# Kernel tuning notes

Hardware: AMD Instinct MI355X
Metric: run time of the kernel (lower is better)

The kernel has to match this reference:

```python
import jax, jax.numpy as jnp
import numpy as np

N = 100000      # nodes (max(content_indices)+1)
E = 1600000     # edges
TXT, VIS = 768, 512
IN = 128        # in_channels (already even)
FEAT = IN + 3   # feature_size = in_channels + 3 (ars)
HID, OUT, CAT = 128, 128, 2
NEG_SLOPE = 0.2


def setup_inputs() -> dict:
    key = jax.random.key(0)
    ks = jax.random.split(key, 20)
    p = lambda k, sh: jax.random.normal(k, sh, jnp.float32) * 0.02
    return {
        "image_features": jax.random.normal(ks[0], (N, VIS), jnp.float32),
        "text_features": jax.random.normal(ks[1], (N, TXT), jnp.float32),
        "content_indices": jnp.arange(N, dtype=jnp.int32),
        "gt_indices": jax.random.randint(ks[2], (N,), 0, 2, jnp.int32),
        "edges": jax.random.randint(ks[3], (E, 2), 0, N, jnp.int32),
        "ars": jax.random.uniform(ks[4], (N, 3), jnp.float32),
        # linear projections
        "Wi": p(ks[5], (VIS, IN // 2)), "bi": jnp.zeros((IN // 2,), jnp.float32),
        "Wt": p(ks[6], (TXT, IN // 2)), "bt": jnp.zeros((IN // 2,), jnp.float32),
        # GATConv layer 0: FEAT -> HID (heads=1)
        "W0": p(ks[7], (FEAT, HID)), "as0": p(ks[8], (HID,)), "ad0": p(ks[9], (HID,)),
        "b0": jnp.zeros((HID,), jnp.float32),
        # GATConv layer 1: HID -> OUT
        "W1": p(ks[10], (HID, OUT)), "as1": p(ks[11], (OUT,)), "ad1": p(ks[12], (OUT,)),
        "b1": jnp.zeros((OUT,), jnp.float32),
        "Wa": p(ks[13], (OUT, CAT)), "ba": jnp.zeros((CAT,), jnp.float32),
        "Wd": p(ks[14], (OUT, CAT)), "bd": jnp.zeros((CAT,), jnp.float32),
    }


def gat_conv(x, src, dst, W, att_src, att_dst, bias):
    """PyG GATConv, heads=1, add_self_loops=True, negative_slope=0.2."""
    h = x @ W                                    # [N, D]
    loop = jnp.arange(N, dtype=src.dtype)
    s = jnp.concatenate([src, loop])             # [E+N]
    d = jnp.concatenate([dst, loop])
    a_s = (h * att_src).sum(-1)                  # [N]
    a_d = (h * att_dst).sum(-1)
    e = jax.nn.leaky_relu(a_s[s] + a_d[d], NEG_SLOPE)   # [E+N]
    # segment softmax over incoming edges of each dst node
    e_max = jax.ops.segment_max(e, d, num_segments=N)
    ee = jnp.exp(e - e_max[d])
    denom = jax.ops.segment_sum(ee, d, num_segments=N)
    alpha = ee / (denom[d] + 1e-16)
    out = jax.ops.segment_sum(h[s] * alpha[:, None], d, num_segments=N)
    return out + bias


def reference(image_features, text_features, content_indices, gt_indices, edges, ars,
              Wi, bi, Wt, bt, W0, as0, ad0, b0, W1, as1, ad1, b1, Wa, ba, Wd, bd):
    img = image_features @ Wi + bi              # [N, IN//2]
    txt = text_features @ Wt + bt               # [N, IN//2]
    inp = jnp.concatenate([img, txt, ars], axis=1)   # [N, FEAT]
    node = jnp.zeros((N, FEAT), jnp.float32).at[content_indices].set(inp)
    node = jax.nn.gelu(node, approximate=False)
    src, dst = edges[:, 0], edges[:, 1]         # edge_index = edges.T
    h = gat_conv(node, src, dst, W0, as0, ad0, b0)
    h = jax.nn.relu(h)                          # PyG GAT inter-layer act
    h = gat_conv(h, src, dst, W1, as1, ad1, b1)
    out = jax.nn.gelu(h, approximate=False)     # [N, OUT]
    angles = out @ Wa + ba                      # [N, CAT]
    dists = out @ Wd + bd
    # per-edge tiny dot products (bmm of [E,1,C] x [E,C,1])
    ap = jnp.sum(angles[src] * angles[dst], axis=-1, keepdims=True)  # [E,1]
    dp = jnp.sum(dists[src] * dists[dst], axis=-1, keepdims=True)
    prediction = jnp.concatenate([ap, dp], axis=-1)   # [E, 2]
    return out, prediction
```

## Files before the change

### kernel.cpp

```cpp
#include <hip/hip_runtime.h>
#include <math.h>

#define N_NODES 100000
#define N_EDGES 1600000
#define FEATP 132
#define HID 128

__device__ __forceinline__ float geluf(float x) {
    return 0.5f * x * (1.0f + erff(x * 0.7071067811865475f));
}
__device__ __forceinline__ float leakyf(float x) {
    return x >= 0.0f ? x : 0.2f * x;
}
__device__ __forceinline__ float wave_reduce_max(float v) {
#pragma unroll
    for (int o = 32; o > 0; o >>= 1) v = fmaxf(v, __shfl_xor(v, o, 64));
    return v;
}
__device__ __forceinline__ float wave_reduce_sum(float v) {
#pragma unroll
    for (int o = 32; o > 0; o >>= 1) v += __shfl_xor(v, o, 64);
    return v;
}

template <int ACT>
__global__ __launch_bounds__(256) void gemm128(
    const float* __restrict__ A, int lda, int M, int K,
    const float* __restrict__ B, int ldb,
    const float* __restrict__ bias,
    float* __restrict__ C, int ldc, int colOff,
    const int* __restrict__ rowIdx)
{
    __shared__ float As[32][132];
    __shared__ float Bs[32][64];
    const int tid = threadIdx.x;
    const int m0 = blockIdx.x * 128;
    const int n0 = blockIdx.y * 64;
    const int tx = tid & 15, ty = tid >> 4;

    const int arow = tid >> 3;
    const int acol = (tid & 7) * 4;
    const int brow = tid >> 4;
    const int bcol = (tid & 15) * 4;

    float4 pa[4], pb[2];
    const int T = (K + 31) / 32;

    auto fetch = [&](int k0) {
#pragma unroll
        for (int i = 0; i < 4; ++i) {
            int row = m0 + i * 32 + arow;
            int k = k0 + acol;
            pa[i] = (row < M && k < K) ? *(const float4*)&A[(size_t)row * lda + k]
                                       : make_float4(0.f, 0.f, 0.f, 0.f);
        }
#pragma unroll
        for (int i = 0; i < 2; ++i) {
            int k = k0 + i * 16 + brow;
            pb[i] = (k < K) ? *(const float4*)&B[(size_t)k * ldb + n0 + bcol]
                            : make_float4(0.f, 0.f, 0.f, 0.f);
        }
    };

    float acc[8][4] = {};
    fetch(0);
    for (int t = 0; t < T; ++t) {
#pragma unroll
        for (int i = 0; i < 4; ++i) {
            int row = i * 32 + arow;
            As[acol + 0][row] = pa[i].x;
            As[acol + 1][row] = pa[i].y;
            As[acol + 2][row] = pa[i].z;
            As[acol + 3][row] = pa[i].w;
        }
#pragma unroll
        for (int i = 0; i < 2; ++i)
            *(float4*)&Bs[i * 16 + brow][bcol] = pb[i];
        __syncthreads();
        if (t + 1 < T) fetch((t + 1) * 32);
#pragma unroll
        for (int kk = 0; kk < 32; ++kk) {
            float4 a0 = *(const float4*)&As[kk][ty * 8];
            float4 a1 = *(const float4*)&As[kk][ty * 8 + 4];
            float4 b  = *(const float4*)&Bs[kk][tx * 4];
            float av[8] = {a0.x, a0.y, a0.z, a0.w, a1.x, a1.y, a1.z, a1.w};
            float bv[4] = {b.x, b.y, b.z, b.w};
#pragma unroll
            for (int i = 0; i < 8; ++i)
#pragma unroll
                for (int j = 0; j < 4; ++j)
                    acc[i][j] = fmaf(av[i], bv[j], acc[i][j]);
        }
        __syncthreads();
    }

#pragma unroll
    for (int i = 0; i < 8; ++i) {
        int row = m0 + ty * 8 + i;
        if (row >= M) continue;
        int orow = rowIdx ? rowIdx[row] : row;
        float4 v;
        float* vp = (float*)&v;
#pragma unroll
        for (int j = 0; j < 4; ++j) {
            float x = acc[i][j];
            if (bias) x += bias[n0 + tx * 4 + j];
            if (ACT == 1) x = geluf(x);
            vp[j] = x;
        }
        *(float4*)&C[(size_t)orow * ldc + colOff + n0 + tx * 4] = v;
    }
}

__global__ void ars_kernel(const float* __restrict__ ars, const int* __restrict__ ci,
                           float* __restrict__ node)
{
    int i = blockIdx.x * blockDim.x + threadIdx.x;
    if (i >= N_NODES * 4) return;
    int n = i >> 2, j = i & 3;
    float v = (j < 3) ? geluf(ars[n * 3 + j]) : 0.0f;
    node[(size_t)ci[n] * FEATP + 128 + j] = v;
}

__global__ void pad_W0(const float* __restrict__ W0, float* __restrict__ W0p)
{
    int i = blockIdx.x * blockDim.x + threadIdx.x;
    if (i >= FEATP * HID) return;
    int r = i >> 7;
    W0p[i] = (r < 131) ? W0[i] : 0.0f;
}

__global__ void hist_dst(const int* __restrict__ edges, int* __restrict__ deg)
{
    int e = blockIdx.x * blockDim.x + threadIdx.x;
    if (e < N_EDGES) atomicAdd(&deg[edges[2 * e + 1]], 1);
}

__global__ __launch_bounds__(1024) void scan_excl(const int* __restrict__ deg,
                                                  int* __restrict__ row_ptr)
{
    __shared__ int sd[1024];
    int tid = threadIdx.x;
    int base = 0;
    for (int start = 0; start < N_NODES; start += 1024) {
        int i = start + tid;
        int v = (i < N_NODES) ? deg[i] : 0;
        sd[tid] = v;
        __syncthreads();
        for (int off = 1; off < 1024; off <<= 1) {
            int t = (tid >= off) ? sd[tid - off] : 0;
            __syncthreads();
            sd[tid] += t;
            __syncthreads();
        }
        if (i < N_NODES) row_ptr[i] = base + sd[tid] - v;
        base += sd[1023];
        __syncthreads();
    }
    if (tid == 0) row_ptr[N_NODES] = base;
}

__global__ void copy_int(const int* __restrict__ src, int* __restrict__ dst, int n)
{
    int i = blockIdx.x * blockDim.x + threadIdx.x;
    if (i < n) dst[i] = src[i];
}

__global__ void scatter_csr(const int* __restrict__ edges, int* __restrict__ cursor,
                            int* __restrict__ csr_src)
{
    int e = blockIdx.x * blockDim.x + threadIdx.x;
    if (e >= N_EDGES) return;
    int s = edges[2 * e], d = edges[2 * e + 1];
    int pos = atomicAdd(&cursor[d], 1);
    csr_src[pos] = s;
}

__global__ __launch_bounds__(256) void attn_scores(
    const float* __restrict__ h, const float* __restrict__ atts,
    const float* __restrict__ attd, float* __restrict__ as_, float* __restrict__ ad_)
{
    int lane = threadIdx.x & 63;
    int node = blockIdx.x * 4 + (threadIdx.x >> 6);
    if (node >= N_NODES) return;
    float h0 = h[(size_t)node * HID + lane];
    float h1 = h[(size_t)node * HID + 64 + lane];
    float s = h0 * atts[lane] + h1 * atts[64 + lane];
    float d = h0 * attd[lane] + h1 * attd[64 + lane];
    s = wave_reduce_sum(s);
    d = wave_reduce_sum(d);
    if (lane == 0) { as_[node] = s; ad_[node] = d; }
}

template <int ACT>
__global__ __launch_bounds__(256) void gat_aggregate(
    const float* __restrict__ h,
    const float* __restrict__ as_, const float* __restrict__ ad_,
    const int* __restrict__ row_ptr, const int* __restrict__ csr_src,
    const float* __restrict__ bias, float* __restrict__ outp)
{
    int lane = threadIdx.x & 63;
    int node = blockIdx.x * 4 + (threadIdx.x >> 6);
    if (node >= N_NODES) return;
    int start = row_ptr[node];
    int deg = row_ptr[node + 1] - start;
    float adn = ad_[node];
    float e_self = leakyf(as_[node] + adn);
    float acc0 = 0.0f, acc1 = 0.0f;
    float m, denom;

    if (deg <= 64) {
        int s = 0;
        float e = -INFINITY;
        if (lane < deg) {
            s = csr_src[start + lane];
            e = leakyf(as_[s] + adn);
        }
        m = fmaxf(wave_reduce_max(e), e_self);
        float w = (lane < deg) ? __expf(e - m) : 0.0f;
        denom = wave_reduce_sum(w) + __expf(e_self - m);
        for (int jj = 0; jj < deg; ++jj) {
            int sj = __shfl(s, jj, 64);
            float wj = __shfl(w, jj, 64);
            acc0 += wj * h[(size_t)sj * HID + lane];
            acc1 += wj * h[(size_t)sj * HID + 64 + lane];
        }
    } else {
        float lm = -INFINITY;
        for (int j = lane; j < deg; j += 64)
            lm = fmaxf(lm, leakyf(as_[csr_src[start + j]] + adn));
        m = fmaxf(wave_reduce_max(lm), e_self);
        float lsum = 0.0f;
        for (int j = lane; j < deg; j += 64)
            lsum += __expf(leakyf(as_[csr_src[start + j]] + adn) - m);
        denom = wave_reduce_sum(lsum) + __expf(e_self - m);
        for (int c0 = 0; c0 < deg; c0 += 64) {
            int j = c0 + lane;
            int s = 0;
            float w = 0.0f;
            if (j < deg) {
                s = csr_src[start + j];
                w = __expf(leakyf(as_[s] + adn) - m);
            }
            int cnt = min(64, deg - c0);
            for (int jj = 0; jj < cnt; ++jj) {
                int sj = __shfl(s, jj, 64);
                float wj = __shfl(w, jj, 64);
                acc0 += wj * h[(size_t)sj * HID + lane];
                acc1 += wj * h[(size_t)sj * HID + 64 + lane];
            }
        }
    }

    float wself = __expf(e_self - m);
    acc0 = (acc0 + wself * h[(size_t)node * HID + lane]) / denom;
    acc1 = (acc1 + wself * h[(size_t)node * HID + 64 + lane]) / denom;
    acc0 += bias[lane];
    acc1 += bias[64 + lane];
    if (ACT == 0) {
        acc0 = fmaxf(acc0, 0.0f);
        acc1 = fmaxf(acc1, 0.0f);
    } else {
        acc0 = geluf(acc0);
        acc1 = geluf(acc1);
    }
    outp[(size_t)node * HID + lane] = acc0;
    outp[(size_t)node * HID + 64 + lane] = acc1;
}

__global__ __launch_bounds__(256) void head_proj(
    const float* __restrict__ outf,
    const float* __restrict__ Wa, const float* __restrict__ ba,
    const float* __restrict__ Wd, const float* __restrict__ bd,
    float* __restrict__ adp)
{
    int lane = threadIdx.x & 63;
    int node = blockIdx.x * 4 + (threadIdx.x >> 6);
    if (node >= N_NODES) return;
    float o0 = outf[(size_t)node * HID + lane];
    float o1 = outf[(size_t)node * HID + 64 + lane];
    float a0 = o0 * Wa[lane * 2] + o1 * Wa[(lane + 64) * 2];
    float a1 = o0 * Wa[lane * 2 + 1] + o1 * Wa[(lane + 64) * 2 + 1];
    float d0 = o0 * Wd[lane * 2] + o1 * Wd[(lane + 64) * 2];
    float d1 = o0 * Wd[lane * 2 + 1] + o1 * Wd[(lane + 64) * 2 + 1];
    a0 = wave_reduce_sum(a0);
    a1 = wave_reduce_sum(a1);
    d0 = wave_reduce_sum(d0);
    d1 = wave_reduce_sum(d1);
    if (lane == 0) {
        float4 v = make_float4(a0 + ba[0], a1 + ba[1], d0 + bd[0], d1 + bd[1]);
        ((float4*)adp)[node] = v;
    }
}

__global__ void edge_pred(const int* __restrict__ edges, const float* __restrict__ adp,
                          float* __restrict__ pred)
{
    int e = blockIdx.x * blockDim.x + threadIdx.x;
    if (e >= N_EDGES) return;
    int s = edges[2 * e], d = edges[2 * e + 1];
    float4 ps = ((const float4*)adp)[s];
    float4 pd = ((const float4*)adp)[d];
    pred[2 * e] = ps.x * pd.x + ps.y * pd.y;
    pred[2 * e + 1] = ps.z * pd.z + ps.w * pd.w;
}

extern "C" void kernel_launch(void* const* d_in, const int* in_sizes, int n_in,
                              void* d_out, int out_size, void* d_ws, size_t ws_size,
                              hipStream_t stream)
{
    const float* imgf = (const float*)d_in[0];
    const float* txtf = (const float*)d_in[1];
    const int* ci     = (const int*)d_in[2];
    const int* edges  = (const int*)d_in[4];
    const float* ars  = (const float*)d_in[5];
    const float* Wi   = (const float*)d_in[6];
    const float* bi   = (const float*)d_in[7];
    const float* Wt   = (const float*)d_in[8];
    const float* bt   = (const float*)d_in[9];
    const float* W0   = (const float*)d_in[10];
    const float* as0  = (const float*)d_in[11];
    const float* ad0  = (const float*)d_in[12];
    const float* b0   = (const float*)d_in[13];
    const float* W1   = (const float*)d_in[14];
    const float* as1  = (const float*)d_in[15];
    const float* ad1  = (const float*)d_in[16];
    const float* b1   = (const float*)d_in[17];
    const float* Wa   = (const float*)d_in[18];
    const float* ba   = (const float*)d_in[19];
    const float* Wd   = (const float*)d_in[20];
    const float* bd   = (const float*)d_in[21];
    (void)in_sizes; (void)n_in; (void)out_size; (void)ws_size;

    float* out0 = (float*)d_out;
    float* pred = out0 + (size_t)N_NODES * HID;

    char* ws = (char*)d_ws;
    size_t off = 0;
    auto alloc = [&](size_t bytes) -> void* {
        void* p = ws + off;
        off += (bytes + 255) & ~(size_t)255;
        return p;
    };
    float* node   = (float*)alloc((size_t)N_NODES * FEATP * 4);
    float* hA     = (float*)alloc((size_t)N_NODES * HID * 4);
    float* as_buf = (float*)alloc((size_t)N_NODES * 4);
    float* ad_buf = (float*)alloc((size_t)N_NODES * 4);
    int* row_ptr  = (int*)alloc((size_t)(N_NODES + 1) * 4);
    int* cursor   = (int*)alloc((size_t)N_NODES * 4);
    int* csr_src  = (int*)alloc((size_t)N_EDGES * 4);
    float* adp    = (float*)alloc((size_t)N_NODES * 4 * 4);
    float* W0p    = (float*)alloc((size_t)FEATP * HID * 4);

    int mtiles = (N_NODES + 127) / 128;
    int nwaveblocks = N_NODES / 4;

    hipMemsetAsync(cursor, 0, (size_t)N_NODES * 4, stream);
    hist_dst<<<(N_EDGES + 255) / 256, 256, 0, stream>>>(edges, cursor);
    scan_excl<<<1, 1024, 0, stream>>>(cursor, row_ptr);
    copy_int<<<(N_NODES + 255) / 256, 256, 0, stream>>>(row_ptr, cursor, N_NODES);
    scatter_csr<<<(N_EDGES + 255) / 256, 256, 0, stream>>>(edges, cursor, csr_src);
    pad_W0<<<(FEATP * HID + 255) / 256, 256, 0, stream>>>(W0, W0p);

    gemm128<1><<<dim3(mtiles, 1), 256, 0, stream>>>(imgf, 512, N_NODES, 512, Wi, 64, bi, node, FEATP, 0, ci);
    gemm128<1><<<dim3(mtiles, 1), 256, 0, stream>>>(txtf, 768, N_NODES, 768, Wt, 64, bt, node, FEATP, 64, ci);
    ars_kernel<<<(N_NODES * 4 + 255) / 256, 256, 0, stream>>>(ars, ci, node);

    gemm128<0><<<dim3(mtiles, 2), 256, 0, stream>>>(node, FEATP, N_NODES, FEATP, W0p, HID, nullptr, hA, HID, 0, nullptr);
    attn_scores<<<nwaveblocks, 256, 0, stream>>>(hA, as0, ad0, as_buf, ad_buf);
    gat_aggregate<0><<<nwaveblocks, 256, 0, stream>>>(hA, as_buf, ad_buf, row_ptr, csr_src, b0, node);

    gemm128<0><<<dim3(mtiles, 2), 256, 0, stream>>>(node, HID, N_NODES, HID, W1, HID, nullptr, hA, HID, 0, nullptr);
    attn_scores<<<nwaveblocks, 256, 0, stream>>>(hA, as1, ad1, as_buf, ad_buf);
    gat_aggregate<1><<<nwaveblocks, 256, 0, stream>>>(hA, as_buf, ad_buf, row_ptr, csr_src, b1, out0);

    head_proj<<<nwaveblocks, 256, 0, stream>>>(out0, Wa, ba, Wd, bd, adp);
    edge_pred<<<(N_EDGES + 255) / 256, 256, 0, stream>>>(edges, adp, pred);
}
```

Baseline: 1.588 ms.

## Replace LDS-tiled GEMM with register-resident B tile and parallelize CSR scan

Replaces the shared-memory tiled SGEMM with a kernel where each wave holds a 64-deep slice of B in registers, one column per lane. Each wave walks 16 rows whose A elements are wave-uniform broadcast loads, which removes LDS staging and barriers. Layer-0 K is padded to 192, with W0 padded in zeros and a zeroed tail on the node buffer. The single-block serial exclusive scan becomes a two-pass multi-block scan using wave shuffles. The GEMM gives up the outer-product reuse of A across columns and depends on how well the uniform A loads are served.

```diff
diff --git a/kernel.cpp b/kernel.cpp
--- a/kernel.cpp
+++ b/kernel.cpp
@@ -4,6 +4,7 @@
 #define N_NODES 100000
 #define N_EDGES 1600000
 #define FEATP 132
+#define KPAD0 192
 #define HID 128
 
 __device__ __forceinline__ float geluf(float x) {
@@ -24,91 +25,55 @@
 }
 
 template <int ACT>
-__global__ __launch_bounds__(256) void gemm128(
+__global__ __launch_bounds__(256, 3) void gemm_rw(
     const float* __restrict__ A, int lda, int M, int K,
     const float* __restrict__ B, int ldb,
     const float* __restrict__ bias,
     float* __restrict__ C, int ldc, int colOff,
     const int* __restrict__ rowIdx)
 {
-    __shared__ float As[32][132];
-    __shared__ float Bs[32][64];
-    const int tid = threadIdx.x;
-    const int m0 = blockIdx.x * 128;
-    const int n0 = blockIdx.y * 64;
-    const int tx = tid & 15, ty = tid >> 4;
-
-    const int arow = tid >> 3;
-    const int acol = (tid & 7) * 4;
-    const int brow = tid >> 4;
-    const int bcol = (tid & 15) * 4;
-
-    float4 pa[4], pb[2];
-    const int T = (K + 31) / 32;
-
-    auto fetch = [&](int k0) {
-#pragma unroll
-        for (int i = 0; i < 4; ++i) {
-            int row = m0 + i * 32 + arow;
-            int k = k0 + acol;
-            pa[i] = (row < M && k < K) ? *(const float4*)&A[(size_t)row * lda + k]
-                                       : make_float4(0.f, 0.f, 0.f, 0.f);
-        }
-#pragma unroll
-        for (int i = 0; i < 2; ++i) {
-            int k = k0 + i * 16 + brow;
-            pb[i] = (k < K) ? *(const float4*)&B[(size_t)k * ldb + n0 + bcol]
-                            : make_float4(0.f, 0.f, 0.f, 0.f);
-        }
-    };
-
-    float acc[8][4] = {};
-    fetch(0);
+    const int lane = threadIdx.x & 63;
+    const int wid  = __builtin_amdgcn_readfirstlane(threadIdx.x >> 6);
+    const int rbase = (blockIdx.x * 4 + wid) * 16;
+    if (rbase >= M) return;
+    const int ncol = blockIdx.y * 64 + lane;
+
+    float acc[16];
+#pragma unroll
+    for (int r = 0; r < 16; ++r) acc[r] = 0.0f;
+
+    const int T = K >> 6;
     for (int t = 0; t < T; ++t) {
-#pragma unroll
-        for (int i = 0; i < 4; ++i) {
-            int row = i * 32 + arow;
-            As[acol + 0][row] = pa[i].x;
-            As[acol + 1][row] = pa[i].y;
-            As[acol + 2][row] = pa[i].z;
-            As[acol + 3][row] = pa[i].w;
-        }
-#pragma unroll
-        for (int i = 0; i < 2; ++i)
-            *(float4*)&Bs[i * 16 + brow][bcol] = pb[i];
-        __syncthreads();
-        if (t + 1 < T) fetch((t + 1) * 32);
-#pragma unroll
-        for (int kk = 0; kk < 32; ++kk) {
-            float4 a0 = *(const float4*)&As[kk][ty * 8];
-            float4 a1 = *(const float4*)&As[kk][ty * 8 + 4];
-            float4 b  = *(const float4*)&Bs[kk][tx * 4];
-            float av[8] = {a0.x, a0.y, a0.z, a0.w, a1.x, a1.y, a1.z, a1.w};
-            float bv[4] = {b.x, b.y, b.z, b.w};
-#pragma unroll
-            for (int i = 0; i < 8; ++i)
-#pragma unroll
-                for (int j = 0; j < 4; ++j)
-                    acc[i][j] = fmaf(av[i], bv[j], acc[i][j]);
-        }
-        __syncthreads();
-    }
-
-#pragma unroll
-    for (int i = 0; i < 8; ++i) {
-        int row = m0 + ty * 8 + i;
-        if (row >= M) continue;
+        const float* __restrict__ bp = B + (size_t)(t << 6) * ldb + ncol;
+        float breg[64];
+#pragma unroll
+        for (int kk = 0; kk < 64; ++kk) breg[kk] = bp[(size_t)kk * ldb];
+#pragma unroll
+        for (int r = 0; r < 16; ++r) {
+            int row = rbase + r;
+            row = row < M ? row : M - 1;
+            const float* __restrict__ ap = A + (size_t)row * lda + (t << 6);
+            float p0 = 0.f, p1 = 0.f, p2 = 0.f, p3 = 0.f;
+#pragma unroll
+            for (int kk = 0; kk < 64; kk += 4) {
+                p0 = fmaf(ap[kk + 0], breg[kk + 0], p0);
+                p1 = fmaf(ap[kk + 1], breg[kk + 1], p1);
+                p2 = fmaf(ap[kk + 2], breg[kk + 2], p2);
+                p3 = fmaf(ap[kk + 3], breg[kk + 3], p3);
+            }
+            acc[r] += (p0 + p1) + (p2 + p3);
+        }
+    }
+
+    const float bv = bias ? bias[blockIdx.y * 64 + lane] : 0.0f;
+#pragma unroll
+    for (int r = 0; r < 16; ++r) {
+        int row = rbase + r;
+        if (row >= M) break;
         int orow = rowIdx ? rowIdx[row] : row;
-        float4 v;
-        float* vp = (float*)&v;
-#pragma unroll
-        for (int j = 0; j < 4; ++j) {
-            float x = acc[i][j];
-            if (bias) x += bias[n0 + tx * 4 + j];
-            if (ACT == 1) x = geluf(x);
-            vp[j] = x;
-        }
-        *(float4*)&C[(size_t)orow * ldc + colOff + n0 + tx * 4] = v;
+        float x = acc[r] + bv;
+        if (ACT == 1) x = geluf(x);
+        C[(size_t)orow * ldc + colOff + blockIdx.y * 64 + lane] = x;
     }
 }
 
@@ -125,7 +90,7 @@
 __global__ void pad_W0(const float* __restrict__ W0, float* __restrict__ W0p)
 {
     int i = blockIdx.x * blockDim.x + threadIdx.x;
-    if (i >= FEATP * HID) return;
+    if (i >= KPAD0 * HID) return;
     int r = i >> 7;
     W0p[i] = (r < 131) ? W0[i] : 0.0f;
 }
@@ -136,28 +101,55 @@
     if (e < N_EDGES) atomicAdd(&deg[edges[2 * e + 1]], 1);
 }
 
-__global__ __launch_bounds__(1024) void scan_excl(const int* __restrict__ deg,
-                                                  int* __restrict__ row_ptr)
-{
-    __shared__ int sd[1024];
+__global__ __launch_bounds__(1024) void scan_local(const int* __restrict__ deg,
+                                                   int* __restrict__ out,
+                                                   int* __restrict__ partials)
+{
+    __shared__ int sw[16];
     int tid = threadIdx.x;
-    int base = 0;
-    for (int start = 0; start < N_NODES; start += 1024) {
-        int i = start + tid;
-        int v = (i < N_NODES) ? deg[i] : 0;
-        sd[tid] = v;
-        __syncthreads();
-        for (int off = 1; off < 1024; off <<= 1) {
-            int t = (tid >= off) ? sd[tid - off] : 0;
-            __syncthreads();
-            sd[tid] += t;
-            __syncthreads();
-        }
-        if (i < N_NODES) row_ptr[i] = base + sd[tid] - v;
-        base += sd[1023];
-        __syncthreads();
-    }
-    if (tid == 0) row_ptr[N_NODES] = base;
+    int gid = blockIdx.x * 1024 + tid;
+    int lane = tid & 63, w = tid >> 6;
+    int v = (gid < N_NODES) ? deg[gid] : 0;
+    int x = v;
+#pragma unroll
+    for (int off = 1; off < 64; off <<= 1) {
+        int t = __shfl_up(x, off, 64);
+        if (lane >= off) x += t;
+    }
+    if (lane == 63) sw[w] = x;
+    __syncthreads();
+    if (tid < 64) {
+        int y = (tid < 16) ? sw[tid] : 0;
+#pragma unroll
+        for (int off = 1; off < 16; off <<= 1) {
+            int t = __shfl_up(y, off, 64);
+            if (tid >= off) y += t;
+        }
+        if (tid < 16) sw[tid] = y;
+    }
+    __syncthreads();
+    int base = (w > 0) ? sw[w - 1] : 0;
+    if (gid < N_NODES) out[gid] = base + x - v;
+    if (tid == 1023) partials[blockIdx.x] = base + x;
+}
+
+__global__ __launch_bounds__(1024) void scan_add(int* __restrict__ row_ptr,
+                                                 const int* __restrict__ partials)
+{
+    __shared__ int soff;
+    int b = blockIdx.x, tid = threadIdx.x;
+    if (tid < 64) {
+        int acc = 0;
+        for (int i = tid; i < b; i += 64) acc += partials[i];
+        acc = (int)wave_reduce_sum((float)0) + acc;
+#pragma unroll
+        for (int o = 32; o > 0; o >>= 1) acc += __shfl_xor(acc, o, 64);
+        if (tid == 0) soff = acc;
+    }
+    __syncthreads();
+    int gid = b * 1024 + tid;
+    if (gid < N_NODES) row_ptr[gid] += soff;
+    if (b == 0 && tid == 0) row_ptr[N_NODES] = N_EDGES;
 }
 
 __global__ void copy_int(const int* __restrict__ src, int* __restrict__ dst, int n)
@@ -342,7 +334,7 @@
         off += (bytes + 255) & ~(size_t)255;
         return p;
     };
-    float* node   = (float*)alloc((size_t)N_NODES * FEATP * 4);
+    float* node   = (float*)alloc((size_t)N_NODES * FEATP * 4 + 1024);
     float* hA     = (float*)alloc((size_t)N_NODES * HID * 4);
     float* as_buf = (float*)alloc((size_t)N_NODES * 4);
     float* ad_buf = (float*)alloc((size_t)N_NODES * 4);
@@ -350,27 +342,31 @@
     int* cursor   = (int*)alloc((size_t)N_NODES * 4);
     int* csr_src  = (int*)alloc((size_t)N_EDGES * 4);
     float* adp    = (float*)alloc((size_t)N_NODES * 4 * 4);
-    float* W0p    = (float*)alloc((size_t)FEATP * HID * 4);
-
-    int mtiles = (N_NODES + 127) / 128;
-    int nwaveblocks = N_NODES / 4;
+    float* W0p    = (float*)alloc((size_t)KPAD0 * HID * 4);
+    int* partials = (int*)alloc(512);
+
+    const int gemm_mblocks = (N_NODES + 63) / 64;
+    const int nwaveblocks = N_NODES / 4;
+    const int scan_blocks = (N_NODES + 1023) / 1024;
 
     hipMemsetAsync(cursor, 0, (size_t)N_NODES * 4, stream);
+    hipMemsetAsync((char*)node + (size_t)N_NODES * FEATP * 4, 0, 1024, stream);
     hist_dst<<<(N_EDGES + 255) / 256, 256, 0, stream>>>(edges, cursor);
-    scan_excl<<<1, 1024, 0, stream>>>(cursor, row_ptr);
+    scan_local<<<scan_blocks, 1024, 0, stream>>>(cursor, row_ptr, partials);
+    scan_add<<<scan_blocks, 1024, 0, stream>>>(row_ptr, partials);
     copy_int<<<(N_NODES + 255) / 256, 256, 0, stream>>>(row_ptr, cursor, N_NODES);
     scatter_csr<<<(N_EDGES + 255) / 256, 256, 0, stream>>>(edges, cursor, csr_src);
-    pad_W0<<<(FEATP * HID + 255) / 256, 256, 0, stream>>>(W0, W0p);
-
-    gemm128<1><<<dim3(mtiles, 1), 256, 0, stream>>>(imgf, 512, N_NODES, 512, Wi, 64, bi, node, FEATP, 0, ci);
-    gemm128<1><<<dim3(mtiles, 1), 256, 0, stream>>>(txtf, 768, N_NODES, 768, Wt, 64, bt, node, FEATP, 64, ci);
+    pad_W0<<<(KPAD0 * HID + 255) / 256, 256, 0, stream>>>(W0, W0p);
+
+    gemm_rw<1><<<dim3(gemm_mblocks, 1), 256, 0, stream>>>(imgf, 512, N_NODES, 512, Wi, 64, bi, node, FEATP, 0, ci);
+    gemm_rw<1><<<dim3(gemm_mblocks, 1), 256, 0, stream>>>(txtf, 768, N_NODES, 768, Wt, 64, bt, node, FEATP, 64, ci);
     ars_kernel<<<(N_NODES * 4 + 255) / 256, 256, 0, stream>>>(ars, ci, node);
 
-    gemm128<0><<<dim3(mtiles, 2), 256, 0, stream>>>(node, FEATP, N_NODES, FEATP, W0p, HID, nullptr, hA, HID, 0, nullptr);
+    gemm_rw<0><<<dim3(gemm_mblocks, 2), 256, 0, stream>>>(node, FEATP, N_NODES, KPAD0, W0p, HID, nullptr, hA, HID, 0, nullptr);
     attn_scores<<<nwaveblocks, 256, 0, stream>>>(hA, as0, ad0, as_buf, ad_buf);
     gat_aggregate<0><<<nwaveblocks, 256, 0, stream>>>(hA, as_buf, ad_buf, row_ptr, csr_src, b0, node);
 
-    gemm128<0><<<dim3(mtiles, 2), 256, 0, stream>>>(node, HID, N_NODES, HID, W1, HID, nullptr, hA, HID, 0, nullptr);
+    gemm_rw<0><<<dim3(gemm_mblocks, 2), 256, 0, stream>>>(node, HID, N_NODES, HID, W1, HID, nullptr, hA, HID, 0, nullptr);
     attn_scores<<<nwaveblocks, 256, 0, stream>>>(hA, as1, ad1, as_buf, ad_buf);
     gat_aggregate<1><<<nwaveblocks, 256, 0, stream>>>(hA, as_buf, ad_buf, row_ptr, csr_src, b1, out0);
 
```

Measured after the change: 2.142 ms. 34.9% more time.
